# Optimization experiments

Hardware: AMD Instinct MI355X
Metric: run time of the kernel (lower is better)

Reference implementation:

```python
import jax, jax.numpy as jnp
import numpy as np

D_MODEL = 1024
D_OUT = 1024
N_EXPERTS = 8
TOP_K = 2


def setup_inputs() -> dict:
    key = jax.random.key(0)
    ks = jax.random.split(key, 5)
    b, t = 4, 4096
    inputs = jax.random.normal(ks[0], (b, t, D_MODEL), dtype=jnp.float32)
    # gate: Linear(input_dim, num_experts) -> weight (E, d), bias (E,)
    Wg = jax.random.normal(ks[1], (N_EXPERTS, D_MODEL), dtype=jnp.float32) / np.sqrt(D_MODEL)
    bg = jnp.zeros((N_EXPERTS,), dtype=jnp.float32)
    # experts: E x Linear(input_dim, output_dim) -> (E, d, f) and (E, f)
    We = jax.random.normal(ks[2], (N_EXPERTS, D_MODEL, D_OUT), dtype=jnp.float32) / np.sqrt(D_MODEL)
    be = jnp.zeros((N_EXPERTS, D_OUT), dtype=jnp.float32)
    return {"inputs": inputs, "Wg": Wg, "bg": bg, "We": We, "be": be}


def reference(inputs, Wg, bg, We, be):
    # gate logits: (b, t, E)
    gate_logits = jnp.einsum('btd,ed->bte', inputs, Wg) + bg
    # top-k per token (values descending, distinct indices) -> (b, t, k)
    topv, topi = jax.lax.top_k(gate_logits, TOP_K)
    gatew = jax.nn.sigmoid(topv).astype(inputs.dtype)            # (b, t, k)
    # scatter the k gate weights into a dense per-expert combine weight (b, t, E)
    onehot = jax.nn.one_hot(topi, N_EXPERTS, dtype=inputs.dtype)  # (b, t, k, E)
    combine = jnp.einsum('btk,btke->bte', gatew, onehot)          # (b, t, E)
    # per-expert linear outputs for all tokens: (b, t, E, f)
    expert_out = jnp.einsum('btd,edf->btef', inputs, We) + be
    # weighted combine over experts (unselected experts have weight 0)
    results = jnp.einsum('bte,btef->btf', combine, expert_out)
    return results
```

## Files before the change

### kernel.cpp

```cpp
#include <hip/hip_runtime.h>
#include <math.h>

#define DM 1024
#define DF 1024
#define NE 8
#define NBIN 16
#define MAXT 136
#define BM 128
#define BN 128
#define BKT 64

typedef __bf16 bf16x8 __attribute__((ext_vector_type(8)));
typedef __bf16 bf16x4 __attribute__((ext_vector_type(4)));
typedef float floatx4 __attribute__((ext_vector_type(4)));

typedef const __attribute__((address_space(1))) unsigned int* gas_t;
typedef __attribute__((address_space(3))) unsigned int* las_t;

__device__ __forceinline__ void ld_lds16(const void* g, void* l) {
    __builtin_amdgcn_global_load_lds((gas_t)g, (las_t)l, 16, 0, 0);
}


__global__ void convert_weT(const float* __restrict__ We, __bf16* __restrict__ WeT) {
    int n  = blockIdx.x * 256 + threadIdx.x;
    int kc = blockIdx.y * 8;
    int e  = blockIdx.z;
    const float* src = We + ((size_t)e << 20) + (size_t)kc * DF + n;
    bf16x8 v;
#pragma unroll
    for (int j = 0; j < 8; ++j) v[j] = (__bf16)src[(size_t)j * DF];
    *(bf16x8*)&WeT[((size_t)e << 20) + (size_t)n * DM + kc] = v;
}

__global__ void gate_kernel(const float4* __restrict__ X4, const float4* __restrict__ Wg4,
                            const float* __restrict__ bg, int* __restrict__ tok_e,
                            float* __restrict__ tok_w, __bf16* __restrict__ Xb, int T) {
    int wid  = threadIdx.x >> 6;
    int lane = threadIdx.x & 63;
    int t = blockIdx.x * 4 + wid;
    if (t >= T) return;
    float acc[NE] = {};
    float4 xs[4];
#pragma unroll
    for (int c = 0; c < 4; ++c) {
        float4 xv = X4[(size_t)t * 256 + c * 64 + lane];
        xs[c] = xv;
#pragma unroll
        for (int e = 0; e < NE; ++e) {
            float4 wv = Wg4[e * 256 + c * 64 + lane];
            acc[e] += xv.x * wv.x + xv.y * wv.y + xv.z * wv.z + xv.w * wv.w;
        }
    }
#pragma unroll
    for (int c = 0; c < 4; ++c) {
        bf16x4 v;
        v[0] = (__bf16)xs[c].x; v[1] = (__bf16)xs[c].y;
        v[2] = (__bf16)xs[c].z; v[3] = (__bf16)xs[c].w;
        *(bf16x4*)&Xb[(size_t)t * DM + c * 256 + lane * 4] = v;
    }
#pragma unroll
    for (int e = 0; e < NE; ++e) {
#pragma unroll
        for (int off = 32; off > 0; off >>= 1)
            acc[e] += __shfl_down(acc[e], off, 64);
    }
    if (lane == 0) {
        float l[NE];
#pragma unroll
        for (int e = 0; e < NE; ++e) l[e] = acc[e] + bg[e];
        int b0 = 0; float v0 = l[0];
        for (int e = 1; e < NE; ++e) if (l[e] > v0) { v0 = l[e]; b0 = e; }
        int b1 = -1; float v1 = -3.4e38f;
        for (int e = 0; e < NE; ++e) if (e != b0 && l[e] > v1) { v1 = l[e]; b1 = e; }
        tok_e[2 * t]     = b0;  tok_e[2 * t + 1] = b1;
        tok_w[2 * t]     = 1.f / (1.f + expf(-v0));
        tok_w[2 * t + 1] = 1.f / (1.f + expf(-v1));
    }
}

__global__ void hist_kernel(const int* __restrict__ tok_e, int* __restrict__ blk_cnt, int n) {
    int b = blockIdx.x, tid = threadIdx.x;
    int idx  = b * 256 + tid;
    int lane = tid & 63, w = tid >> 6;
    int bin = (idx < n) ? ((idx & 1) * NE + tok_e[idx]) : -1;
    __shared__ int wc[4][NBIN];
#pragma unroll
    for (int bx = 0; bx < NBIN; ++bx) {
        unsigned long long m = __ballot(bin == bx);
        if (lane == 0) wc[w][bx] = (int)__popcll(m);
    }
    __syncthreads();
    if (tid < NBIN) blk_cnt[b * NBIN + tid] = wc[0][tid] + wc[1][tid] + wc[2][tid] + wc[3][tid];
}

__global__ void scan_kernel(const int* __restrict__ blk_cnt, int* __restrict__ blk_base,
                            int4* __restrict__ wl, int* __restrict__ ntiles, int NB) {
    __shared__ int c[2048];
    __shared__ int tot[NBIN], base[NBIN];
    int tid = threadIdx.x;
    for (int i = tid; i < NB * NBIN; i += 256) c[i] = blk_cnt[i];
    __syncthreads();
    if (tid < NBIN) {
        int s = 0;
        for (int b = 0; b < NB; ++b) s += c[b * NBIN + tid];
        tot[tid] = s;
    }
    __syncthreads();
    if (tid == 0) {
        int s = 0;
        for (int b = 0; b < NBIN; ++b) { base[b] = s; s += tot[b]; }
    }
    __syncthreads();
    if (tid < NBIN) {
        int run = base[tid];
        for (int b = 0; b < NB; ++b) { int v = c[b * NBIN + tid]; c[b * NBIN + tid] = run; run += v; }
    }
    __syncthreads();
    for (int i = tid; i < NB * NBIN; i += 256) blk_base[i] = c[i];
    if (tid == 0) {
        for (int p = 0; p < 2; ++p) {
            int nt = 0;
            for (int e = 0; e < NE; ++e) {
                int bin = p * NE + e;
                int cnt = tot[bin], sg = base[bin];
                for (int r0 = 0; r0 < cnt; r0 += BM)
                    wl[p * MAXT + nt++] = make_int4(e, r0, sg, cnt);
            }
            ntiles[p] = nt;
        }
    }
}

__global__ void scatter_kernel(const int* __restrict__ tok_e, const float* __restrict__ tok_w,
                               const int* __restrict__ blk_base, int* __restrict__ gath_tok,
                               float* __restrict__ gath_w, int n) {
    int b = blockIdx.x, tid = threadIdx.x;
    int idx  = b * 256 + tid;
    int lane = tid & 63, w = tid >> 6;
    bool act = idx < n;
    int bin = act ? ((idx & 1) * NE + tok_e[idx]) : -1;
    __shared__ int wc[4][NBIN], wb[4][NBIN];
    int myrank = 0;
#pragma unroll
    for (int bx = 0; bx < NBIN; ++bx) {
        unsigned long long m = __ballot(bin == bx);
        if (lane == 0) wc[w][bx] = (int)__popcll(m);
        if (bin == bx) myrank = (int)__popcll(m & ((1ull << lane) - 1ull));
    }
    __syncthreads();
    if (tid < NBIN) {
        int run = blk_base[b * NBIN + tid];
#pragma unroll
        for (int wv = 0; wv < 4; ++wv) { wb[wv][tid] = run; run += wc[wv][tid]; }
    }
    __syncthreads();
    if (act) {
        int pos = wb[w][bin] + myrank;
        gath_tok[pos] = idx >> 1;
        gath_w[pos]   = tok_w[idx];
    }
}

template <bool ACC>
__global__ __launch_bounds__(256) void expert_gemm_mfma(
        const __bf16* __restrict__ Xb, const __bf16* __restrict__ WeT,
        const float* __restrict__ be, const int4* __restrict__ wl,
        const int* __restrict__ ntiles, const int* __restrict__ gtok,
        const float* __restrict__ gw, float* __restrict__ out) {
    int sw = (blockIdx.x & 7) * MAXT + (blockIdx.x >> 3);
    int tix  = sw >> 3;
    int col0 = (sw & 7) * BN;
    if (tix >= ntiles[0]) return;
    int4 ent = wl[tix];
    int e = ent.x, row0 = ent.y, seg = ent.z, n_e = ent.w;

    __shared__ __align__(16) char smem_raw[64 * 1024];
    __bf16* As0 = (__bf16*)(smem_raw);
    __bf16* As1 = (__bf16*)(smem_raw + 16384);
    __bf16* Bs0 = (__bf16*)(smem_raw + 32768);
    __bf16* Bs1 = (__bf16*)(smem_raw + 49152);
    __shared__ int   s_tok[BM];
    __shared__ float s_w[BM];

    int tid = threadIdx.x;
    if (tid < BM) {
        int gr = row0 + tid;
        s_tok[tid] = (gr < n_e) ? gtok[seg + gr] : gtok[seg];
        s_w[tid]   = (gr < n_e) ? gw[seg + gr]   : 0.f;
    }
    __syncthreads();

    int lane = tid & 63, w = tid >> 6;
    int lr = lane >> 3;
    int kc = (lane & 7) ^ lr;

    const __bf16* aptr[4];
    const __bf16* bptr[4];
#pragma unroll
    for (int p = 0; p < 4; ++p) {
        int r = p * 32 + w * 8 + lr;
        aptr[p] = Xb + (size_t)s_tok[r] * DM + kc * 8;
        bptr[p] = WeT + ((size_t)e << 20) + (size_t)(col0 + r) * DM + kc * 8;
    }

    int wr = (w >> 1) * 64, wcc = (w & 1) * 64;
    int m16 = lane & 15, q = lane >> 4;
    int rsw = m16 & 7;

    floatx4 acc[4][4] = {};

    auto stage = [&](int koff, __bf16* AD, __bf16* BD) {
#pragma unroll
        for (int p = 0; p < 4; ++p) ld_lds16(aptr[p] + koff, &AD[(p * 4 + w) * 512]);
#pragma unroll
        for (int p = 0; p < 4; ++p) ld_lds16(bptr[p] + koff, &BD[(p * 4 + w) * 512]);
    };
    auto compute = [&](const __bf16* AS, const __bf16* BS) {
#pragma unroll
        for (int kt = 0; kt < 2; ++kt) {
            bf16x8 af[4], bfr[4];
#pragma unroll
            for (int i = 0; i < 4; ++i)
                af[i] = *(const bf16x8*)&AS[(wr + i * 16 + m16) * 64 + ((kt * 4 + q) ^ rsw) * 8];
#pragma unroll
            for (int i = 0; i < 4; ++i)
                bfr[i] = *(const bf16x8*)&BS[(wcc + i * 16 + m16) * 64 + ((kt * 4 + q) ^ rsw) * 8];
#pragma unroll
            for (int i = 0; i < 4; ++i)
#pragma unroll
                for (int j = 0; j < 4; ++j)
                    acc[i][j] = __builtin_amdgcn_mfma_f32_16x16x32_bf16(af[i], bfr[j], acc[i][j], 0, 0, 0);
        }
    };

    stage(0, As0, Bs0);
    __syncthreads();

    for (int k0 = 0; k0 < DM; k0 += 2 * BKT) {
        stage(k0 + BKT, As1, Bs1);
        compute(As0, Bs0);
        __syncthreads();
        if (k0 + 2 * BKT < DM) stage(k0 + 2 * BKT, As0, Bs0);
        compute(As1, Bs1);
        __syncthreads();
    }

    float* Cs = (float*)smem_raw;
#pragma unroll
    for (int j = 0; j < 4; ++j) {
#pragma unroll
        for (int i = 0; i < 4; ++i) {
#pragma unroll
            for (int rg = 0; rg < 4; ++rg) {
                int rl = wr + i * 16 + q * 4 + rg;
                int cl = wcc + j * 16 + m16;
                int quad = (cl >> 2) ^ (rl & 31);
                Cs[rl * 128 + quad * 4 + (cl & 3)] = acc[i][j][rg];
            }
        }
    }
    __syncthreads();

#pragma unroll
    for (int rh = 0; rh < 2; ++rh) {
        int rr = w * 32 + rh * 16 + (lane >> 2);
        int gr2 = row0 + rr;
        if (gr2 < n_e) {
            int tok = s_tok[rr];
            float wgt = s_w[rr];
            float* orow = out + (size_t)tok * DF + col0;
            const float* brow = be + e * DF + col0;
#pragma unroll
            for (int k = 0; k < 8; ++k) {
                int cq = k * 4 + (lane & 3);
                int c4 = cq * 4;
                floatx4 v  = *(const floatx4*)&Cs[rr * 128 + ((cq ^ (rr & 31)) * 4)];
                floatx4 bv = *(const floatx4*)&brow[c4];
                floatx4 r;
#pragma unroll
                for (int z = 0; z < 4; ++z) r[z] = wgt * (v[z] + bv[z]);
                if (ACC) {
                    floatx4 o = *(const floatx4*)&orow[c4];
#pragma unroll
                    for (int z = 0; z < 4; ++z) r[z] += o[z];
                }
                *(floatx4*)&orow[c4] = r;
            }
        }
    }
}

extern "C" void kernel_launch(void* const* d_in, const int* in_sizes, int n_in,
                              void* d_out, int out_size, void* d_ws, size_t ws_size,
                              hipStream_t stream) {
    const float* x  = (const float*)d_in[0];
    const float* Wg = (const float*)d_in[1];
    const float* bg = (const float*)d_in[2];
    const float* We = (const float*)d_in[3];
    const float* be = (const float*)d_in[4];
    float* out = (float*)d_out;

    int T = in_sizes[0] / DM;
    int n_slots = 2 * T;
    int NB = (n_slots + 255) / 256;

    char* ws = (char*)d_ws;
    size_t xb_bytes  = (size_t)T * DM * 2;
    size_t weT_bytes = (size_t)NE * DM * DF * 2;
    __bf16* Xb  = (__bf16*)ws;
    __bf16* WeT = (__bf16*)(ws + xb_bytes);
    char* rt = ws + xb_bytes + weT_bytes;
    int*   ntiles    = (int*)(rt + 0);
    int4*  wl        = (int4*)(rt + 64);
    int*   blk_cnt   = (int*)(rt + 64 + 2 * MAXT * 16);
    int*   blk_base  = (int*)((char*)blk_cnt + (size_t)NB * NBIN * 4);
    int*   tok_e     = (int*)((char*)blk_base + (size_t)NB * NBIN * 4);
    float* tok_w     = (float*)((char*)tok_e + (size_t)n_slots * 4);
    int*   gath_tok  = (int*)((char*)tok_w + (size_t)n_slots * 4);
    float* gath_w    = (float*)((char*)gath_tok + (size_t)n_slots * 4);

    convert_weT<<<dim3(DF / 256, DM / 8, NE), 256, 0, stream>>>(We, WeT);
    gate_kernel<<<(T + 3) / 4, 256, 0, stream>>>((const float4*)x, (const float4*)Wg,
                                                 bg, tok_e, tok_w, Xb, T);
    hist_kernel<<<NB, 256, 0, stream>>>(tok_e, blk_cnt, n_slots);
    scan_kernel<<<1, 256, 0, stream>>>(blk_cnt, blk_base, wl, ntiles, NB);
    scatter_kernel<<<NB, 256, 0, stream>>>(tok_e, tok_w, blk_base, gath_tok, gath_w, n_slots);

    expert_gemm_mfma<false><<<MAXT * 8, 256, 0, stream>>>(Xb, WeT, be, wl, ntiles,
                                                          gath_tok, gath_w, out);
    expert_gemm_mfma<true><<<MAXT * 8, 256, 0, stream>>>(Xb, WeT, be, wl + MAXT, ntiles + 1,
                                                         gath_tok, gath_w, out);
}
```

Measured before the change: 315.7 us.

## Switch expert GEMM to 128x64 tiles with 4-stage async LDS pipeline

Shrinks the expert GEMM tile from 128x128 with BK=64 double buffering to 128x64 with BK=32. Global-to-LDS loads now run through a four-buffer ring with explicit vmcnt waits and raw barriers, so three stages are in flight while one is computed. The grid doubles to keep the swizzled block mapping consistent and to give more blocks and occupancy. The cost is lower arithmetic intensity per tile, since A rows are reloaded twice as often, plus more barriers per K step.

```diff
diff --git a/kernel.cpp b/kernel.cpp
--- a/kernel.cpp
+++ b/kernel.cpp
@@ -7,8 +7,9 @@
 #define NBIN 16
 #define MAXT 136
 #define BM 128
-#define BN 128
-#define BKT 64
+#define BN 64
+#define BKT 32
+#define NT 32
 
 typedef __bf16 bf16x8 __attribute__((ext_vector_type(8)));
 typedef __bf16 bf16x4 __attribute__((ext_vector_type(4)));
@@ -20,6 +21,11 @@
 __device__ __forceinline__ void ld_lds16(const void* g, void* l) {
     __builtin_amdgcn_global_load_lds((gas_t)g, (las_t)l, 16, 0, 0);
 }
+
+#define WAITVM(N) asm volatile("s_waitcnt vmcnt(" #N ")" ::: "memory")
+#define BARRIER() do { asm volatile("" ::: "memory"); \
+                       __builtin_amdgcn_s_barrier(); \
+                       asm volatile("" ::: "memory"); } while (0)
 
 
 __global__ void convert_weT(const float* __restrict__ We, __bf16* __restrict__ WeT) {
@@ -168,18 +174,17 @@
         const float* __restrict__ be, const int4* __restrict__ wl,
         const int* __restrict__ ntiles, const int* __restrict__ gtok,
         const float* __restrict__ gw, float* __restrict__ out) {
-    int sw = (blockIdx.x & 7) * MAXT + (blockIdx.x >> 3);
-    int tix  = sw >> 3;
-    int col0 = (sw & 7) * BN;
+    int sw = (blockIdx.x & 7) * (2 * MAXT) + (blockIdx.x >> 3);
+    int tix  = sw >> 4;
+    int col0 = (sw & 15) * BN;
     if (tix >= ntiles[0]) return;
     int4 ent = wl[tix];
     int e = ent.x, row0 = ent.y, seg = ent.z, n_e = ent.w;
 
-    __shared__ __align__(16) char smem_raw[64 * 1024];
-    __bf16* As0 = (__bf16*)(smem_raw);
-    __bf16* As1 = (__bf16*)(smem_raw + 16384);
-    __bf16* Bs0 = (__bf16*)(smem_raw + 32768);
-    __bf16* Bs1 = (__bf16*)(smem_raw + 49152);
+    __shared__ __align__(16) char smem[49152];
+    __bf16* Asb = (__bf16*)smem;
+    __bf16* Bsb = (__bf16*)(smem + 32768);
+    float*  Cs  = (float*)smem;
     __shared__ int   s_tok[BM];
     __shared__ float s_w[BM];
 
@@ -192,75 +197,73 @@
     __syncthreads();
 
     int lane = tid & 63, w = tid >> 6;
-    int lr = lane >> 3;
-    int kc = (lane & 7) ^ lr;
-
-    const __bf16* aptr[4];
-    const __bf16* bptr[4];
-#pragma unroll
-    for (int p = 0; p < 4; ++p) {
-        int r = p * 32 + w * 8 + lr;
-        aptr[p] = Xb + (size_t)s_tok[r] * DM + kc * 8;
-        bptr[p] = WeT + ((size_t)e << 20) + (size_t)(col0 + r) * DM + kc * 8;
-    }
-
-    int wr = (w >> 1) * 64, wcc = (w & 1) * 64;
-    int m16 = lane & 15, q = lane >> 4;
-    int rsw = m16 & 7;
-
-    floatx4 acc[4][4] = {};
-
-    auto stage = [&](int koff, __bf16* AD, __bf16* BD) {
-#pragma unroll
-        for (int p = 0; p < 4; ++p) ld_lds16(aptr[p] + koff, &AD[(p * 4 + w) * 512]);
-#pragma unroll
-        for (int p = 0; p < 4; ++p) ld_lds16(bptr[p] + koff, &BD[(p * 4 + w) * 512]);
-    };
-    auto compute = [&](const __bf16* AS, const __bf16* BS) {
-#pragma unroll
-        for (int kt = 0; kt < 2; ++kt) {
-            bf16x8 af[4], bfr[4];
-#pragma unroll
-            for (int i = 0; i < 4; ++i)
-                af[i] = *(const bf16x8*)&AS[(wr + i * 16 + m16) * 64 + ((kt * 4 + q) ^ rsw) * 8];
-#pragma unroll
-            for (int i = 0; i < 4; ++i)
-                bfr[i] = *(const bf16x8*)&BS[(wcc + i * 16 + m16) * 64 + ((kt * 4 + q) ^ rsw) * 8];
-#pragma unroll
-            for (int i = 0; i < 4; ++i)
-#pragma unroll
-                for (int j = 0; j < 4; ++j)
-                    acc[i][j] = __builtin_amdgcn_mfma_f32_16x16x32_bf16(af[i], bfr[j], acc[i][j], 0, 0, 0);
-        }
-    };
-
-    stage(0, As0, Bs0);
-    __syncthreads();
-
-    for (int k0 = 0; k0 < DM; k0 += 2 * BKT) {
-        stage(k0 + BKT, As1, Bs1);
-        compute(As0, Bs0);
-        __syncthreads();
-        if (k0 + 2 * BKT < DM) stage(k0 + 2 * BKT, As0, Bs0);
-        compute(As1, Bs1);
-        __syncthreads();
-    }
-
-    float* Cs = (float*)smem_raw;
-#pragma unroll
-    for (int j = 0; j < 4; ++j) {
+    int rsub = lane >> 2;
+    int kc   = (lane & 3) ^ ((lane >> 3) & 3);
+
+    const __bf16* aptr0 = Xb + (size_t)s_tok[w * 16 + rsub] * DM + kc * 8;
+    const __bf16* aptr1 = Xb + (size_t)s_tok[(4 + w) * 16 + rsub] * DM + kc * 8;
+    const __bf16* bptr  = WeT + ((size_t)e << 20)
+                        + (size_t)(col0 + w * 16 + rsub) * DM + kc * 8;
+
+    int wr  = (w >> 1) * 64;
+    int wcc = (w & 1) * 32;
+    int m16 = lane & 15, q4 = lane >> 4;
+    int ccu = q4 ^ ((m16 >> 1) & 3);
+
+    floatx4 acc[4][2] = {};
+
+#define STAGE(B, KS) do { \
+    ld_lds16(aptr0 + (KS) * BKT, Asb + (B) * 4096 + w * 512); \
+    ld_lds16(aptr1 + (KS) * BKT, Asb + (B) * 4096 + (4 + w) * 512); \
+    ld_lds16(bptr  + (KS) * BKT, Bsb + (B) * 2048 + w * 512); } while (0)
+
+#define COMP(B) do { \
+    bf16x8 af[4], bfr[2]; \
+    _Pragma("unroll") \
+    for (int i = 0; i < 4; ++i) \
+        af[i] = *(const bf16x8*)&Asb[(B) * 4096 + (wr + i * 16 + m16) * 32 + ccu * 8]; \
+    _Pragma("unroll") \
+    for (int j = 0; j < 2; ++j) \
+        bfr[j] = *(const bf16x8*)&Bsb[(B) * 2048 + (wcc + j * 16 + m16) * 32 + ccu * 8]; \
+    _Pragma("unroll") \
+    for (int i = 0; i < 4; ++i) \
+        _Pragma("unroll") \
+        for (int j = 0; j < 2; ++j) \
+            acc[i][j] = __builtin_amdgcn_mfma_f32_16x16x32_bf16(af[i], bfr[j], acc[i][j], 0, 0, 0); \
+    } while (0)
+
+    STAGE(0, 0); STAGE(1, 1); STAGE(2, 2);
+    WAITVM(6);
+    BARRIER();
+
+    for (int kk = 0; kk < NT - 4; kk += 4) {
+        COMP(0); BARRIER(); STAGE(3, kk + 3); WAITVM(6); BARRIER();
+        COMP(1); BARRIER(); STAGE(0, kk + 4); WAITVM(6); BARRIER();
+        COMP(2); BARRIER(); STAGE(1, kk + 5); WAITVM(6); BARRIER();
+        COMP(3); BARRIER(); STAGE(2, kk + 6); WAITVM(6); BARRIER();
+    }
+    COMP(0); BARRIER(); STAGE(3, NT - 1); WAITVM(6); BARRIER();
+    COMP(1); BARRIER(); WAITVM(3); BARRIER();
+    COMP(2); BARRIER(); WAITVM(0); BARRIER();
+    COMP(3); BARRIER();
+
+#undef STAGE
+#undef COMP
+
+#pragma unroll
+    for (int j = 0; j < 2; ++j) {
 #pragma unroll
         for (int i = 0; i < 4; ++i) {
 #pragma unroll
             for (int rg = 0; rg < 4; ++rg) {
-                int rl = wr + i * 16 + q * 4 + rg;
+                int rl = wr + i * 16 + q4 * 4 + rg;
                 int cl = wcc + j * 16 + m16;
-                int quad = (cl >> 2) ^ (rl & 31);
-                Cs[rl * 128 + quad * 4 + (cl & 3)] = acc[i][j][rg];
+                int cq = (cl >> 2) ^ (rl & 15);
+                Cs[rl * 64 + cq * 4 + (cl & 3)] = acc[i][j][rg];
             }
         }
     }
-    __syncthreads();
+    BARRIER();
 
 #pragma unroll
     for (int rh = 0; rh < 2; ++rh) {
@@ -272,10 +275,10 @@
             float* orow = out + (size_t)tok * DF + col0;
             const float* brow = be + e * DF + col0;
 #pragma unroll
-            for (int k = 0; k < 8; ++k) {
-                int cq = k * 4 + (lane & 3);
-                int c4 = cq * 4;
-                floatx4 v  = *(const floatx4*)&Cs[rr * 128 + ((cq ^ (rr & 31)) * 4)];
+            for (int kq = 0; kq < 4; ++kq) {
+                int cq_log = kq * 4 + (lane & 3);
+                int c4 = cq_log * 4;
+                floatx4 v  = *(const floatx4*)&Cs[rr * 64 + ((cq_log ^ (rr & 15)) * 4)];
                 floatx4 bv = *(const floatx4*)&brow[c4];
                 floatx4 r;
 #pragma unroll
@@ -327,8 +330,8 @@
     scan_kernel<<<1, 256, 0, stream>>>(blk_cnt, blk_base, wl, ntiles, NB);
     scatter_kernel<<<NB, 256, 0, stream>>>(tok_e, tok_w, blk_base, gath_tok, gath_w, n_slots);
 
-    expert_gemm_mfma<false><<<MAXT * 8, 256, 0, stream>>>(Xb, WeT, be, wl, ntiles,
+    expert_gemm_mfma<false><<<MAXT * 16, 256, 0, stream>>>(Xb, WeT, be, wl, ntiles,
+                                                           gath_tok, gath_w, out);
+    expert_gemm_mfma<true><<<MAXT * 16, 256, 0, stream>>>(Xb, WeT, be, wl + MAXT, ntiles + 1,
                                                           gath_tok, gath_w, out);
-    expert_gemm_mfma<true><<<MAXT * 8, 256, 0, stream>>>(Xb, WeT, be, wl + MAXT, ntiles + 1,
-                                                         gath_tok, gath_w, out);
-}
+}
```

New measurement: 310.9 us. No clear change (-1.5%).
